# Kernel optimization log

Hardware: AMD Instinct MI355X
Metric: run time of the kernel (lower is better)

Reference implementation:

```python
import jax, jax.numpy as jnp
import numpy as np

N_POINTS = 300000
N_PAIRS = 100000  # rulebook pairs per kernel offset
K_OFFSETS = 27    # 3x3x3 kernel
C_IN, C_OUT = 32, 64
GROUPS = 8
EPS = 1e-5
NEG_SLOPE = 0.01


def setup_inputs() -> dict:
    key = jax.random.key(0)
    k1, k2, k3, k4 = jax.random.split(key, 4)
    feats = jax.random.normal(k1, (N_POINTS, C_IN), dtype=jnp.float32)
    weight = jax.random.normal(k2, (K_OFFSETS, C_IN, C_OUT), dtype=jnp.float32) * (1.0 / np.sqrt(C_IN * K_OFFSETS))
    gamma = jnp.ones((C_OUT,), dtype=jnp.float32)
    beta = jnp.zeros((C_OUT,), dtype=jnp.float32)
    in_idx = jax.random.randint(k3, (K_OFFSETS, N_PAIRS), 0, N_POINTS, dtype=jnp.int64)
    out_idx = jax.random.randint(k4, (K_OFFSETS, N_PAIRS), 0, N_POINTS, dtype=jnp.int64)
    return {"feats": feats, "weight": weight, "gamma": gamma, "beta": beta,
            "in_idx": in_idx, "out_idx": out_idx}


def reference(feats, weight, gamma, beta, in_idx, out_idx):
    # Sparse 3D conv via rulebook: gather -> per-offset matmul -> scatter-add
    gathered = feats[in_idx]                       # [K, P, C_in]
    y = jnp.einsum('kpi,kio->kpo', gathered, weight)  # [K, P, C_out]
    out = jnp.zeros((feats.shape[0], weight.shape[2]), feats.dtype)
    out = out.at[out_idx.reshape(-1)].add(y.reshape(-1, weight.shape[2]))
    # GroupNorm(8, C_out): stats over all points and channels within each group
    N, C = out.shape
    xg = out.reshape(N, GROUPS, C // GROUPS)
    mean = jnp.mean(xg, axis=(0, 2), keepdims=True)
    var = jnp.var(xg, axis=(0, 2), keepdims=True)
    xn = ((xg - mean) * jax.lax.rsqrt(var + EPS)).reshape(N, C)
    xn = xn * gamma + beta
    # LeakyReLU (default negative_slope = 0.01)
    return jnp.where(xn >= 0, xn, NEG_SLOPE * xn)
```

## Files before the change

### kernel.cpp

```cpp
#include <hip/hip_runtime.h>

#define NPTS   300000
#define NPAIRS 100000
#define KOFF   27
#define CIN    32
#define COUT   64
#define NGROUP 8
#define EPSV   1e-5f
#define SLOPE  0.01f

#define PAIRS_PER_BLOCK 256
#define BLOCKS_PER_K ((NPAIRS + PAIRS_PER_BLOCK - 1) / PAIRS_PER_BLOCK)

__global__ __launch_bounds__(256) void zero_kernel(float4* __restrict__ out4, int n4,
                                                   float* __restrict__ stats) {
    int i = blockIdx.x * blockDim.x + threadIdx.x;
    if (i < n4) out4[i] = make_float4(0.f, 0.f, 0.f, 0.f);
    if (blockIdx.x == 0 && threadIdx.x < 16) stats[threadIdx.x] = 0.f;
}

__global__ __launch_bounds__(256) void conv_kernel(
    const float* __restrict__ feats, const float* __restrict__ weight,
    const int* __restrict__ in_idx, const int* __restrict__ out_idx,
    float* __restrict__ out)
{
    const int lane = threadIdx.x & 63;
    const int wave = threadIdx.x >> 6;
    const int k     = blockIdx.x / BLOCKS_PER_K;
    const int pair0 = (blockIdx.x % BLOCKS_PER_K) * PAIRS_PER_BLOCK;

    float w[CIN];
    const float* wk = weight + k * (CIN * COUT) + lane;
#pragma unroll
    for (int i = 0; i < CIN; ++i) w[i] = wk[i * COUT];
#pragma unroll
    for (int i = 0; i < CIN; ++i) asm volatile("" : "+v"(w[i]));

    const int per_wave = PAIRS_PER_BLOCK / 4;
    int p    = pair0 + wave * per_wave;
    int pend = p + per_wave;
    if (pend > NPAIRS) pend = NPAIRS;

    const int* ii = in_idx  + k * NPAIRS;
    const int* oi = out_idx + k * NPAIRS;

    for (; p < pend; ++p) {
        int rin  = __builtin_amdgcn_readfirstlane(ii[p]);
        int rout = __builtin_amdgcn_readfirstlane(oi[p]);
        const float* frow = feats + (size_t)rin * CIN;
        float a0 = 0.f, a1 = 0.f, a2 = 0.f, a3 = 0.f;
#pragma unroll
        for (int i = 0; i < CIN; i += 4) {
            a0 = fmaf(frow[i],     w[i],     a0);
            a1 = fmaf(frow[i + 1], w[i + 1], a1);
            a2 = fmaf(frow[i + 2], w[i + 2], a2);
            a3 = fmaf(frow[i + 3], w[i + 3], a3);
        }
        atomicAdd(out + (size_t)rout * COUT + lane, (a0 + a1) + (a2 + a3));
    }
}

__global__ __launch_bounds__(256) void stats_kernel(const float4* __restrict__ out4,
                                                    float* __restrict__ stats) {
    const int tid  = blockIdx.x * 256 + threadIdx.x;
    const int ntid = gridDim.x * 256;
    const int n4   = NPTS * COUT / 4;

    float s = 0.f, ss = 0.f;
    for (int i = tid; i < n4; i += ntid) {
        float4 v = out4[i];
        s  += v.x + v.y + v.z + v.w;
        ss += v.x * v.x + v.y * v.y + v.z * v.z + v.w * v.w;
    }
    s  += __shfl_xor(s,  1, 64);  ss += __shfl_xor(ss,  1, 64);
    s  += __shfl_xor(s, 16, 64);  ss += __shfl_xor(ss, 16, 64);
    s  += __shfl_xor(s, 32, 64);  ss += __shfl_xor(ss, 32, 64);

    __shared__ float sm_s[4][NGROUP];
    __shared__ float sm_ss[4][NGROUP];
    const int lane = threadIdx.x & 63;
    const int wv   = threadIdx.x >> 6;
    if (lane < 16 && (lane & 1) == 0) {
        sm_s [wv][lane >> 1] = s;
        sm_ss[wv][lane >> 1] = ss;
    }
    __syncthreads();
    if (threadIdx.x < NGROUP) {
        float ts = 0.f, tss = 0.f;
#pragma unroll
        for (int wvi = 0; wvi < 4; ++wvi) { ts += sm_s[wvi][threadIdx.x]; tss += sm_ss[wvi][threadIdx.x]; }
        atomicAdd(stats + threadIdx.x,          ts);
        atomicAdd(stats + NGROUP + threadIdx.x, tss);
    }
}

__global__ __launch_bounds__(256) void norm_kernel(float4* __restrict__ out4, int n4,
                                                   const float* __restrict__ stats,
                                                   const float* __restrict__ gamma,
                                                   const float* __restrict__ beta) {
    int i = blockIdx.x * blockDim.x + threadIdx.x;
    if (i >= n4) return;
    int c0 = (i & 15) * 4;
    int g  = c0 >> 3;
    const float cnt = (float)NPTS * (COUT / NGROUP);
    float mean = stats[g] / cnt;
    float var  = stats[8 + g] / cnt - mean * mean;
    float inv  = rsqrtf(var + EPSV);
    float4 v  = out4[i];
    float4 ga = *(const float4*)(gamma + c0);
    float4 be = *(const float4*)(beta  + c0);
    float x;
    x = (v.x - mean) * inv * ga.x + be.x; v.x = x >= 0.f ? x : SLOPE * x;
    x = (v.y - mean) * inv * ga.y + be.y; v.y = x >= 0.f ? x : SLOPE * x;
    x = (v.z - mean) * inv * ga.z + be.z; v.z = x >= 0.f ? x : SLOPE * x;
    x = (v.w - mean) * inv * ga.w + be.w; v.w = x >= 0.f ? x : SLOPE * x;
    out4[i] = v;
}

extern "C" void kernel_launch(void* const* d_in, const int* in_sizes, int n_in,
                              void* d_out, int out_size, void* d_ws, size_t ws_size,
                              hipStream_t stream) {
    const float* feats  = (const float*)d_in[0];
    const float* weight = (const float*)d_in[1];
    const float* gamma  = (const float*)d_in[2];
    const float* beta   = (const float*)d_in[3];
    const int*   in_idx = (const int*)d_in[4];
    const int*   out_idx= (const int*)d_in[5];
    float* out   = (float*)d_out;
    float* stats = (float*)d_ws;

    int n4 = out_size / 4;
    int zb = (n4 + 255) / 256;

    zero_kernel<<<zb, 256, 0, stream>>>((float4*)out, n4, stats);
    conv_kernel<<<KOFF * BLOCKS_PER_K, 256, 0, stream>>>(feats, weight, in_idx, out_idx, out);
    stats_kernel<<<2048, 256, 0, stream>>>((const float4*)out, stats);
    norm_kernel<<<zb, 256, 0, stream>>>((float4*)out, n4, stats, gamma, beta);
}
```

Measured before the change: 761.0 us.

## Batch-load rulebook indices per wave and double-buffer feature row gathers

Each lane now loads one in/out index for the wave's 64 pairs up front and broadcasts them with shuffles, replacing two dependent scalar index loads per pair. Feature rows are fetched as float4 vectors into two alternating register buffers, so the gather for pair j+2 is issued while pair j is computed and atomically added. This is meant to hide gather latency in the latency-bound conv loop, at the cost of extra VGPRs for the two 32-float buffers. The asm volatile register pinning of the weights is dropped, and waves with no pairs now exit early.

```diff
diff --git a/kernel.cpp b/kernel.cpp
--- a/kernel.cpp
+++ b/kernel.cpp
@@ -29,34 +29,52 @@
     const int k     = blockIdx.x / BLOCKS_PER_K;
     const int pair0 = (blockIdx.x % BLOCKS_PER_K) * PAIRS_PER_BLOCK;
 
+    const int p0 = pair0 + wave * 64;
+    if (p0 >= NPAIRS) return;
+    int n = NPAIRS - p0; if (n > 64) n = 64;
+
     float w[CIN];
     const float* wk = weight + k * (CIN * COUT) + lane;
 #pragma unroll
     for (int i = 0; i < CIN; ++i) w[i] = wk[i * COUT];
-#pragma unroll
-    for (int i = 0; i < CIN; ++i) asm volatile("" : "+v"(w[i]));
-
-    const int per_wave = PAIRS_PER_BLOCK / 4;
-    int p    = pair0 + wave * per_wave;
-    int pend = p + per_wave;
-    if (pend > NPAIRS) pend = NPAIRS;
 
     const int* ii = in_idx  + k * NPAIRS;
     const int* oi = out_idx + k * NPAIRS;
+    int pidx = p0 + lane; if (pidx >= NPAIRS) pidx = NPAIRS - 1;
+    const int rinv  = ii[pidx];
+    const int routv = oi[pidx];
 
-    for (; p < pend; ++p) {
-        int rin  = __builtin_amdgcn_readfirstlane(ii[p]);
-        int rout = __builtin_amdgcn_readfirstlane(oi[p]);
-        const float* frow = feats + (size_t)rin * CIN;
+    float4 A[8], B[8];
+
+    auto loadrow = [&](int j, float4* R) {
+        int r = __shfl(rinv, j, 64);
+        const float4* fr = (const float4*)(feats + (size_t)r * CIN);
+#pragma unroll
+        for (int q = 0; q < 8; ++q) R[q] = fr[q];
+    };
+    auto compute = [&](const float4* R, int j) {
+        int rout = __shfl(routv, j, 64);
         float a0 = 0.f, a1 = 0.f, a2 = 0.f, a3 = 0.f;
 #pragma unroll
-        for (int i = 0; i < CIN; i += 4) {
-            a0 = fmaf(frow[i],     w[i],     a0);
-            a1 = fmaf(frow[i + 1], w[i + 1], a1);
-            a2 = fmaf(frow[i + 2], w[i + 2], a2);
-            a3 = fmaf(frow[i + 3], w[i + 3], a3);
+        for (int q = 0; q < 8; ++q) {
+            a0 = fmaf(R[q].x, w[4 * q + 0], a0);
+            a1 = fmaf(R[q].y, w[4 * q + 1], a1);
+            a2 = fmaf(R[q].z, w[4 * q + 2], a2);
+            a3 = fmaf(R[q].w, w[4 * q + 3], a3);
         }
         atomicAdd(out + (size_t)rout * COUT + lane, (a0 + a1) + (a2 + a3));
+    };
+
+    loadrow(0, A);
+    if (n > 1) loadrow(1, B);
+    int j = 0;
+    while (true) {
+        compute(A, j);
+        if (j + 2 < n) loadrow(j + 2, A);
+        ++j; if (j >= n) break;
+        compute(B, j);
+        if (j + 2 < n) loadrow(j + 2, B);
+        ++j; if (j >= n) break;
     }
 }
 
```

New measurement: 944.7 us. 24.1% more time.

## Stage gathered feature rows in LDS with per-lane loads before wave-wide matmul

Applied to the files above, without the earlier changes.

Each wave now loads its 64 pair indices in parallel, one per lane, and each lane copies one input feature row into shared memory with float4 loads. The compute loop then reads rows from LDS as broadcast float4s and takes the output index via a shuffle, instead of serial readfirstlane index loads and scalar global loads per pair. This is meant to remove serialized global index-load latency and expose memory-level parallelism for the random gathers. In exchange it uses about 36 KB of LDS per block, which may reduce occupancy, and it drops the asm barrier that pinned the weights in registers.

```diff
diff --git a/kernel.cpp b/kernel.cpp
--- a/kernel.cpp
+++ b/kernel.cpp
@@ -24,38 +24,55 @@
     const int* __restrict__ in_idx, const int* __restrict__ out_idx,
     float* __restrict__ out)
 {
+    __shared__ float rows[4][64][36];
     const int lane = threadIdx.x & 63;
-    const int wave = threadIdx.x >> 6;
+    const int wv   = threadIdx.x >> 6;
     const int k     = blockIdx.x / BLOCKS_PER_K;
-    const int pair0 = (blockIdx.x % BLOCKS_PER_K) * PAIRS_PER_BLOCK;
+    const int pair0 = (blockIdx.x % BLOCKS_PER_K) * PAIRS_PER_BLOCK + wv * 64;
+    if (pair0 >= NPAIRS) return;
+    int n = NPAIRS - pair0; if (n > 64) n = 64;
 
     float w[CIN];
     const float* wk = weight + k * (CIN * COUT) + lane;
 #pragma unroll
     for (int i = 0; i < CIN; ++i) w[i] = wk[i * COUT];
-#pragma unroll
-    for (int i = 0; i < CIN; ++i) asm volatile("" : "+v"(w[i]));
-
-    const int per_wave = PAIRS_PER_BLOCK / 4;
-    int p    = pair0 + wave * per_wave;
-    int pend = p + per_wave;
-    if (pend > NPAIRS) pend = NPAIRS;
 
     const int* ii = in_idx  + k * NPAIRS;
     const int* oi = out_idx + k * NPAIRS;
 
-    for (; p < pend; ++p) {
-        int rin  = __builtin_amdgcn_readfirstlane(ii[p]);
-        int rout = __builtin_amdgcn_readfirstlane(oi[p]);
-        const float* frow = feats + (size_t)rin * CIN;
+    const int myp   = pair0 + ((lane < n) ? lane : (n - 1));
+    const int routv = oi[myp];
+
+    if (lane < n) {
+        const int rin = ii[myp];
+        const float4* fr = (const float4*)(feats + (size_t)rin * CIN);
+        float4* dst = (float4*)&rows[wv][lane][0];
+#pragma unroll
+        for (int q = 0; q < 8; ++q) dst[q] = fr[q];
+    }
+
+    for (int j = 0; j < n; ++j) {
+        const int rout = __shfl(routv, j, 64);
+        const float4* fr4 = (const float4*)&rows[wv][j][0];
+        float4 r0 = fr4[0], r1 = fr4[1], r2 = fr4[2], r3 = fr4[3];
+        float4 r4 = fr4[4], r5 = fr4[5], r6 = fr4[6], r7 = fr4[7];
         float a0 = 0.f, a1 = 0.f, a2 = 0.f, a3 = 0.f;
-#pragma unroll
-        for (int i = 0; i < CIN; i += 4) {
-            a0 = fmaf(frow[i],     w[i],     a0);
-            a1 = fmaf(frow[i + 1], w[i + 1], a1);
-            a2 = fmaf(frow[i + 2], w[i + 2], a2);
-            a3 = fmaf(frow[i + 3], w[i + 3], a3);
-        }
+        a0 = fmaf(r0.x, w[0],  a0); a1 = fmaf(r0.y, w[1],  a1);
+        a2 = fmaf(r0.z, w[2],  a2); a3 = fmaf(r0.w, w[3],  a3);
+        a0 = fmaf(r1.x, w[4],  a0); a1 = fmaf(r1.y, w[5],  a1);
+        a2 = fmaf(r1.z, w[6],  a2); a3 = fmaf(r1.w, w[7],  a3);
+        a0 = fmaf(r2.x, w[8],  a0); a1 = fmaf(r2.y, w[9],  a1);
+        a2 = fmaf(r2.z, w[10], a2); a3 = fmaf(r2.w, w[11], a3);
+        a0 = fmaf(r3.x, w[12], a0); a1 = fmaf(r3.y, w[13], a1);
+        a2 = fmaf(r3.z, w[14], a2); a3 = fmaf(r3.w, w[15], a3);
+        a0 = fmaf(r4.x, w[16], a0); a1 = fmaf(r4.y, w[17], a1);
+        a2 = fmaf(r4.z, w[18], a2); a3 = fmaf(r4.w, w[19], a3);
+        a0 = fmaf(r5.x, w[20], a0); a1 = fmaf(r5.y, w[21], a1);
+        a2 = fmaf(r5.z, w[22], a2); a3 = fmaf(r5.w, w[23], a3);
+        a0 = fmaf(r6.x, w[24], a0); a1 = fmaf(r6.y, w[25], a1);
+        a2 = fmaf(r6.z, w[26], a2); a3 = fmaf(r6.w, w[27], a3);
+        a0 = fmaf(r7.x, w[28], a0); a1 = fmaf(r7.y, w[29], a1);
+        a2 = fmaf(r7.z, w[30], a2); a3 = fmaf(r7.w, w[31], a3);
         atomicAdd(out + (size_t)rout * COUT + lane, (a0 + a1) + (a2 + a3));
     }
 }
```

Result: faster. 743.2 us (-2.3%).
